# Performance work log

Hardware: AMD Instinct MI355X
Metric: run time of the kernel (lower is better)

Reference implementation:

```python
import jax, jax.numpy as jnp
import numpy as np

B, T, C, H = 4, 2048, 1024, 16
D = C // H  # head_dim = 64
SCALE = 1.0 / np.sqrt(D).astype(np.float32)


def setup_inputs() -> dict:
    key = jax.random.key(0)
    k1, k2, k3 = jax.random.split(key, 3)
    x = jax.random.normal(k1, (B, T, C), dtype=jnp.float32)
    Wqkv = jax.random.normal(k2, (C, 3 * C), dtype=jnp.float32) * (1.0 / np.sqrt(C))
    Wo = jax.random.normal(k3, (C, C), dtype=jnp.float32) * (1.0 / np.sqrt(C))
    bo = jnp.zeros((C,), dtype=jnp.float32)
    # causal mask, broadcastable [1,1,T,T]; positions where mask==0 get -inf
    mask = jnp.tril(jnp.ones((T, T), dtype=jnp.int32))[None, None]
    return {"x": x, "mask": mask, "Wqkv": Wqkv, "Wo": Wo, "bo": bo}


def reference(x, mask, Wqkv, Wo, bo):
    Bx, Tx, Cx = x.shape
    qkv = x @ Wqkv                               # [B, T, 3C]
    q, k, v = jnp.split(qkv, 3, axis=-1)
    # [B, T, C] -> [B, H, T, D]
    def heads(t):
        return t.reshape(Bx, Tx, H, D).transpose(0, 2, 1, 3)
    q, k, v = heads(q), heads(k), heads(v)
    scores = jnp.einsum('bhqd,bhkd->bhqk', q, k) * SCALE   # [B, H, T, T]
    scores = jnp.where(mask == 0, -jnp.inf, scores)
    attn = jax.nn.softmax(scores, axis=-1)
    out = jnp.einsum('bhqk,bhkd->bhqd', attn, v)           # [B, H, T, D]
    out = out.transpose(0, 2, 1, 3).reshape(Bx, Tx, Cx)    # [B, T, C]
    return out @ Wo + bo
```

## Files before the change

### kernel.cpp

```cpp
#include <hip/hip_runtime.h>

typedef __attribute__((ext_vector_type(8))) short short8;
typedef __attribute__((ext_vector_type(4))) float f32x4;
typedef __attribute__((ext_vector_type(4))) unsigned short ushort4v;

#define QK_PRESCALE 0.18033688011112043f
#define DEFER_THR 11.5f

__device__ __forceinline__ unsigned short f2bf(float f) {
    union { float f; unsigned int u; } v; v.f = f;
    unsigned int r = v.u + 0x7FFFu + ((v.u >> 16) & 1u);
    return (unsigned short)(r >> 16);
}

__global__ __launch_bounds__(256) void cvt_bf16(const float* __restrict__ in,
                                                unsigned short* __restrict__ out, int n) {
    int i = (blockIdx.x * 256 + threadIdx.x) * 4;
    if (i >= n) return;
    f32x4 v = *(const f32x4*)(in + i);
    ushort4v o;
    o[0] = f2bf(v[0]); o[1] = f2bf(v[1]); o[2] = f2bf(v[2]); o[3] = f2bf(v[3]);
    *(ushort4v*)(out + i) = o;
}

__global__ __launch_bounds__(256) void transpose_cvt(const float* __restrict__ W,
                                                     unsigned short* __restrict__ WT,
                                                     int Kd, int Nd) {
    __shared__ float tile[32][33];
    int n0 = blockIdx.x * 32, k0 = blockIdx.y * 32;
    int tx = threadIdx.x, ty = threadIdx.y;
    #pragma unroll
    for (int i = 0; i < 4; ++i)
        tile[ty + i * 8][tx] = W[(size_t)(k0 + ty + i * 8) * Nd + n0 + tx];
    __syncthreads();
    #pragma unroll
    for (int i = 0; i < 4; ++i) {
        int r = ty + i * 8;
        WT[(size_t)(n0 + r) * Kd + k0 + tx] = f2bf(tile[tx][r]);
    }
}

#define AS1U(p) ((const __attribute__((address_space(1))) unsigned int*)(p))
#define AS3U(p) ((__attribute__((address_space(3))) unsigned int*)(p))

template<int BIAS, int OUTBF16, int QSCALE>
__global__ __launch_bounds__(256) void gemm_bt(const unsigned short* __restrict__ A,
                                               const unsigned short* __restrict__ BT,
                                               void* __restrict__ Cv,
                                               const float* __restrict__ bias,
                                               int M, int N, int K) {
    __shared__ unsigned short As[128 * 32];
    __shared__ unsigned short Bs[128 * 32];
    int tid = threadIdx.x;
    int l = tid & 63, l15 = l & 15, l4 = l >> 4;
    int w = tid >> 6, wm = w >> 1, wn = w & 1;
    int bm = blockIdx.x, bn = blockIdx.y;

    f32x4 acc[4][4];
    #pragma unroll
    for (int mt = 0; mt < 4; ++mt)
        #pragma unroll
        for (int nt = 0; nt < 4; ++nt)
            acc[mt][nt] = (f32x4){0.f, 0.f, 0.f, 0.f};

    int srow = tid >> 2;
    int skk  = (tid & 3) * 8;

    const unsigned short* Ab = A  + (size_t)(bm * 128) * K;
    const unsigned short* Bb = BT + (size_t)(bn * 128) * K;

    for (int kt = 0; kt < K; kt += 32) {
        __syncthreads();
        __builtin_amdgcn_global_load_lds(AS1U(Ab + (size_t)srow        * K + kt + skk), AS3U(&As[tid * 8]),         16, 0, 0);
        __builtin_amdgcn_global_load_lds(AS1U(Ab + (size_t)(srow + 64) * K + kt + skk), AS3U(&As[(256 + tid) * 8]), 16, 0, 0);
        __builtin_amdgcn_global_load_lds(AS1U(Bb + (size_t)srow        * K + kt + skk), AS3U(&Bs[tid * 8]),         16, 0, 0);
        __builtin_amdgcn_global_load_lds(AS1U(Bb + (size_t)(srow + 64) * K + kt + skk), AS3U(&Bs[(256 + tid) * 8]), 16, 0, 0);
        __syncthreads();

        short8 av[4], bv[4];
        #pragma unroll
        for (int mt = 0; mt < 4; ++mt)
            av[mt] = *(const short8*)&As[(wm * 64 + mt * 16 + l15) * 32 + l4 * 8];
        #pragma unroll
        for (int nt = 0; nt < 4; ++nt)
            bv[nt] = *(const short8*)&Bs[(wn * 64 + nt * 16 + l15) * 32 + l4 * 8];
        #pragma unroll
        for (int mt = 0; mt < 4; ++mt)
            #pragma unroll
            for (int nt = 0; nt < 4; ++nt)
                acc[mt][nt] = __builtin_amdgcn_mfma_f32_16x16x32_bf16(av[mt], bv[nt], acc[mt][nt], 0, 0, 0);
    }

    #pragma unroll
    for (int mt = 0; mt < 4; ++mt) {
        #pragma unroll
        for (int r = 0; r < 4; ++r) {
            int row = bm * 128 + wm * 64 + mt * 16 + l4 * 4 + r;
            #pragma unroll
            for (int nt = 0; nt < 4; ++nt) {
                int col = bn * 128 + wn * 64 + nt * 16 + l15;
                float vv = acc[mt][nt][r];
                if (BIAS) vv += bias[col];
                if (QSCALE && col < 1024) vv *= QK_PRESCALE;
                if (OUTBF16) ((unsigned short*)Cv)[(size_t)row * N + col] = f2bf(vv);
                else         ((float*)Cv)[(size_t)row * N + col] = vv;
            }
        }
    }
}

__device__ __forceinline__ int swz64(int row, int e) {
    return row * 64 + (e ^ ((row & 7) << 3));
}

__global__ __launch_bounds__(256) void flash_attn(const unsigned short* __restrict__ qk,
                                                  const unsigned short* __restrict__ vt,
                                                  unsigned short* __restrict__ ao) {
    int nid = (blockIdx.x & 7) * 128 + (blockIdx.x >> 3);
    int pr = nid & 15;
    int bh = nid >> 4;
    int b = bh >> 4, h = bh & 15;
    int tid = threadIdx.x;
    int w = tid >> 6, l = tid & 63, l15 = l & 15, l4 = l >> 4;

    __shared__ unsigned short Ks[2][4096];
    __shared__ unsigned short Vs[2][4096];
    __shared__ unsigned short Ps[4096];

    const size_t qkbase = (size_t)b * 2048 * 2048;

    int c0i = w * 128 + l;
    int row0 = c0i >> 3, sub0 = c0i & 7;
    int c1i = c0i + 64;
    int row1 = c1i >> 3, sub1 = c1i & 7;

    const unsigned short* Kp0b = qk + qkbase + 1024 + h * 64 + (size_t)row0 * 2048 + 8 * (sub0 ^ (row0 & 7));
    const unsigned short* Kp1b = qk + qkbase + 1024 + h * 64 + (size_t)row1 * 2048 + 8 * (sub1 ^ (row1 & 7));
    const unsigned short* Vp0b = vt + (size_t)(h * 64 + row0) * 8192 + (size_t)b * 2048 + 8 * (sub0 ^ (row0 & 7));
    const unsigned short* Vp1b = vt + (size_t)(h * 64 + row1) * 8192 + (size_t)b * 2048 + 8 * (sub1 ^ (row1 & 7));

    #define STAGE(buf, kvb_)                                                                        \
        do {                                                                                        \
            size_t koff = (size_t)(kvb_) * (64 * 2048);                                             \
            int    voff = (kvb_) * 64;                                                              \
            __builtin_amdgcn_global_load_lds(AS1U(Kp0b + koff), AS3U(&Ks[buf][w * 1024]),       16, 0, 0); \
            __builtin_amdgcn_global_load_lds(AS1U(Kp1b + koff), AS3U(&Ks[buf][w * 1024 + 512]), 16, 0, 0); \
            __builtin_amdgcn_global_load_lds(AS1U(Vp0b + voff), AS3U(&Vs[buf][w * 1024]),       16, 0, 0); \
            __builtin_amdgcn_global_load_lds(AS1U(Vp1b + voff), AS3U(&Vs[buf][w * 1024 + 512]), 16, 0, 0); \
        } while (0)

    #pragma unroll
    for (int t = 0; t < 2; ++t) {
        int qt = t ? (31 - pr) : pr;

        int qrow = qt * 64 + w * 16 + l15;
        const unsigned short* qp = qk + qkbase + (size_t)qrow * 2048 + h * 64 + l4 * 8;
        short8 qa0 = *(const short8*)(qp);
        short8 qa1 = *(const short8*)(qp + 32);

        float m[4], ll[4];
        f32x4 oacc[4];
        #pragma unroll
        for (int r = 0; r < 4; ++r) { m[r] = -__builtin_inff(); ll[r] = 0.f; }
        #pragma unroll
        for (int dt = 0; dt < 4; ++dt) oacc[dt] = (f32x4){0.f, 0.f, 0.f, 0.f};

        STAGE(0, 0);
        __syncthreads();

        int cur = 0;
        for (int kvb = 0; kvb <= qt; ++kvb) {
            if (kvb < qt) STAGE(cur ^ 1, kvb + 1);

            f32x4 sacc[4];
            __builtin_amdgcn_s_setprio(1);
            #pragma unroll
            for (int kvt = 0; kvt < 4; ++kvt) {
                short8 k0v = *(const short8*)&Ks[cur][swz64(kvt * 16 + l15, l4 * 8)];
                short8 k1v = *(const short8*)&Ks[cur][swz64(kvt * 16 + l15, 32 + l4 * 8)];
                sacc[kvt] = (f32x4){0.f, 0.f, 0.f, 0.f};
                sacc[kvt] = __builtin_amdgcn_mfma_f32_16x16x32_bf16(qa0, k0v, sacc[kvt], 0, 0, 0);
                sacc[kvt] = __builtin_amdgcn_mfma_f32_16x16x32_bf16(qa1, k1v, sacc[kvt], 0, 0, 0);
            }
            __builtin_amdgcn_s_setprio(0);

            if (kvb == qt) {
                #pragma unroll
                for (int kvt = 0; kvt < 4; ++kvt)
                    #pragma unroll
                    for (int r = 0; r < 4; ++r) {
                        int ql = w * 16 + l4 * 4 + r;
                        int kl = kvt * 16 + l15;
                        if (kl > ql) sacc[kvt][r] = -__builtin_inff();
                    }
            }

            #pragma unroll
            for (int r = 0; r < 4; ++r) {
                float tmax = fmaxf(fmaxf(sacc[0][r], sacc[1][r]), fmaxf(sacc[2][r], sacc[3][r]));
                tmax = fmaxf(tmax, __shfl_xor(tmax, 1));
                tmax = fmaxf(tmax, __shfl_xor(tmax, 2));
                tmax = fmaxf(tmax, __shfl_xor(tmax, 4));
                tmax = fmaxf(tmax, __shfl_xor(tmax, 8));
                bool skip = (tmax <= m[r] + DEFER_THR);
                float mn = skip ? m[r] : tmax;
                float rsum = 0.f;
                #pragma unroll
                for (int kvt = 0; kvt < 4; ++kvt) {
                    float p = exp2f(sacc[kvt][r] - mn);
                    sacc[kvt][r] = p;
                    rsum += p;
                }
                rsum += __shfl_xor(rsum, 1);
                rsum += __shfl_xor(rsum, 2);
                rsum += __shfl_xor(rsum, 4);
                rsum += __shfl_xor(rsum, 8);
                if (skip) {
                    ll[r] += rsum;
                } else {
                    float alpha = exp2f(m[r] - mn);
                    ll[r] = ll[r] * alpha + rsum;
                    m[r] = mn;
                    #pragma unroll
                    for (int dt = 0; dt < 4; ++dt) oacc[dt][r] *= alpha;
                }
            }

            #pragma unroll
            for (int kvt = 0; kvt < 4; ++kvt)
                #pragma unroll
                for (int r = 0; r < 4; ++r)
                    Ps[w * 1024 + swz64(l4 * 4 + r, kvt * 16 + l15)] = f2bf(sacc[kvt][r]);
            short8 pa0 = *(const short8*)&Ps[w * 1024 + swz64(l15, l4 * 8)];
            short8 pa1 = *(const short8*)&Ps[w * 1024 + swz64(l15, 32 + l4 * 8)];

            __builtin_amdgcn_s_setprio(1);
            #pragma unroll
            for (int dt = 0; dt < 4; ++dt) {
                short8 vb0 = *(const short8*)&Vs[cur][swz64(dt * 16 + l15, l4 * 8)];
                short8 vb1 = *(const short8*)&Vs[cur][swz64(dt * 16 + l15, 32 + l4 * 8)];
                oacc[dt] = __builtin_amdgcn_mfma_f32_16x16x32_bf16(pa0, vb0, oacc[dt], 0, 0, 0);
                oacc[dt] = __builtin_amdgcn_mfma_f32_16x16x32_bf16(pa1, vb1, oacc[dt], 0, 0, 0);
            }
            __builtin_amdgcn_s_setprio(0);

            __syncthreads();
            cur ^= 1;
        }

        #pragma unroll
        for (int r = 0; r < 4; ++r) {
            float inv = 1.0f / ll[r];
            int row = qt * 64 + w * 16 + l4 * 4 + r;
            unsigned short* op = ao + ((size_t)b * 2048 + row) * 1024 + h * 64;
            #pragma unroll
            for (int dt = 0; dt < 4; ++dt)
                op[dt * 16 + l15] = f2bf(oacc[dt][r] * inv);
        }
    }
    #undef STAGE
}

extern "C" void kernel_launch(void* const* d_in, const int* in_sizes, int n_in,
                              void* d_out, int out_size, void* d_ws, size_t ws_size,
                              hipStream_t stream) {
    const float* x    = (const float*)d_in[0];
    const float* Wqkv = (const float*)d_in[2];
    const float* Wo   = (const float*)d_in[3];
    const float* bo   = (const float*)d_in[4];
    float* out = (float*)d_out;

    char* ws = (char*)d_ws;
    unsigned short* xb    = (unsigned short*)(ws);
    unsigned short* wqkvt = (unsigned short*)(ws + 16777216);
    unsigned short* wot   = (unsigned short*)(ws + 23068672);
    unsigned short* qkb   = (unsigned short*)(ws + 25165824);
    unsigned short* vtb   = (unsigned short*)(ws + 58720256);
    unsigned short* ao    = (unsigned short*)(ws + 75497472);

    cvt_bf16<<<8192, 256, 0, stream>>>(x, xb, 8192 * 1024);
    transpose_cvt<<<dim3(96, 32), dim3(32, 8), 0, stream>>>(Wqkv, wqkvt, 1024, 3072);
    transpose_cvt<<<dim3(32, 32), dim3(32, 8), 0, stream>>>(Wo, wot, 1024, 1024);

    gemm_bt<0, 1, 1><<<dim3(64, 16), 256, 0, stream>>>(xb, wqkvt, (void*)qkb, nullptr, 8192, 2048, 1024);
    gemm_bt<0, 1, 0><<<dim3(8, 64), 256, 0, stream>>>(wqkvt + (size_t)2048 * 1024, xb, (void*)vtb, nullptr, 1024, 8192, 1024);

    flash_attn<<<dim3(1024), 256, 0, stream>>>(qkb, vtb, ao);

    gemm_bt<1, 0, 0><<<dim3(64, 8), 256, 0, stream>>>(ao, wot, (void*)out, bo, 8192, 1024, 1024);
}
```

Before: 395.7 us.

## Compute transposed S tile so each lane owns one query row in softmax

Swaps the MFMA operands in the QK^T product so the score tile comes out transposed, with each lane holding a single query row. Row max and row sum then need only two cross-lane shuffles instead of four per row, and the running max and sum become scalars. The P tile is written to LDS with 4-wide vector stores instead of scalar stores. The output rescale now needs a shuffle to fetch each row's alpha, and that is done only when some lane's max changed.

```diff
diff --git a/kernel.cpp b/kernel.cpp
--- a/kernel.cpp
+++ b/kernel.cpp
@@ -1,6 +1,7 @@
 #include <hip/hip_runtime.h>
 
 typedef __attribute__((ext_vector_type(8))) short short8;
+typedef __attribute__((ext_vector_type(4))) short short4v;
 typedef __attribute__((ext_vector_type(4))) float f32x4;
 typedef __attribute__((ext_vector_type(4))) unsigned short ushort4v;
 
@@ -158,10 +159,8 @@
         short8 qa0 = *(const short8*)(qp);
         short8 qa1 = *(const short8*)(qp + 32);
 
-        float m[4], ll[4];
+        float mrow = -__builtin_inff(), llrow = 0.f;
         f32x4 oacc[4];
-        #pragma unroll
-        for (int r = 0; r < 4; ++r) { m[r] = -__builtin_inff(); ll[r] = 0.f; }
         #pragma unroll
         for (int dt = 0; dt < 4; ++dt) oacc[dt] = (f32x4){0.f, 0.f, 0.f, 0.f};
 
@@ -179,58 +178,68 @@
                 short8 k0v = *(const short8*)&Ks[cur][swz64(kvt * 16 + l15, l4 * 8)];
                 short8 k1v = *(const short8*)&Ks[cur][swz64(kvt * 16 + l15, 32 + l4 * 8)];
                 sacc[kvt] = (f32x4){0.f, 0.f, 0.f, 0.f};
-                sacc[kvt] = __builtin_amdgcn_mfma_f32_16x16x32_bf16(qa0, k0v, sacc[kvt], 0, 0, 0);
-                sacc[kvt] = __builtin_amdgcn_mfma_f32_16x16x32_bf16(qa1, k1v, sacc[kvt], 0, 0, 0);
+                sacc[kvt] = __builtin_amdgcn_mfma_f32_16x16x32_bf16(k0v, qa0, sacc[kvt], 0, 0, 0);
+                sacc[kvt] = __builtin_amdgcn_mfma_f32_16x16x32_bf16(k1v, qa1, sacc[kvt], 0, 0, 0);
             }
             __builtin_amdgcn_s_setprio(0);
 
             if (kvb == qt) {
+                int ql = w * 16 + l15;
                 #pragma unroll
                 for (int kvt = 0; kvt < 4; ++kvt)
                     #pragma unroll
                     for (int r = 0; r < 4; ++r) {
-                        int ql = w * 16 + l4 * 4 + r;
-                        int kl = kvt * 16 + l15;
+                        int kl = kvt * 16 + l4 * 4 + r;
                         if (kl > ql) sacc[kvt][r] = -__builtin_inff();
                     }
             }
 
-            #pragma unroll
-            for (int r = 0; r < 4; ++r) {
-                float tmax = fmaxf(fmaxf(sacc[0][r], sacc[1][r]), fmaxf(sacc[2][r], sacc[3][r]));
-                tmax = fmaxf(tmax, __shfl_xor(tmax, 1));
-                tmax = fmaxf(tmax, __shfl_xor(tmax, 2));
-                tmax = fmaxf(tmax, __shfl_xor(tmax, 4));
-                tmax = fmaxf(tmax, __shfl_xor(tmax, 8));
-                bool skip = (tmax <= m[r] + DEFER_THR);
-                float mn = skip ? m[r] : tmax;
-                float rsum = 0.f;
+            float tmax = sacc[0][0];
+            #pragma unroll
+            for (int kvt = 0; kvt < 4; ++kvt)
                 #pragma unroll
-                for (int kvt = 0; kvt < 4; ++kvt) {
+                for (int r = 0; r < 4; ++r)
+                    tmax = fmaxf(tmax, sacc[kvt][r]);
+            tmax = fmaxf(tmax, __shfl_xor(tmax, 16));
+            tmax = fmaxf(tmax, __shfl_xor(tmax, 32));
+
+            bool skip = (tmax <= mrow + DEFER_THR);
+            float mn = skip ? mrow : tmax;
+            float alphaL = skip ? 1.f : exp2f(mrow - mn);
+
+            float rsum = 0.f;
+            #pragma unroll
+            for (int kvt = 0; kvt < 4; ++kvt)
+                #pragma unroll
+                for (int r = 0; r < 4; ++r) {
                     float p = exp2f(sacc[kvt][r] - mn);
                     sacc[kvt][r] = p;
                     rsum += p;
                 }
-                rsum += __shfl_xor(rsum, 1);
-                rsum += __shfl_xor(rsum, 2);
-                rsum += __shfl_xor(rsum, 4);
-                rsum += __shfl_xor(rsum, 8);
-                if (skip) {
-                    ll[r] += rsum;
-                } else {
-                    float alpha = exp2f(m[r] - mn);
-                    ll[r] = ll[r] * alpha + rsum;
-                    m[r] = mn;
+            rsum += __shfl_xor(rsum, 16);
+            rsum += __shfl_xor(rsum, 32);
+
+            llrow = llrow * alphaL + rsum;
+            mrow = mn;
+
+            if (__any(!skip)) {
+                #pragma unroll
+                for (int r = 0; r < 4; ++r) {
+                    float aO = __shfl(alphaL, l4 * 4 + r);
                     #pragma unroll
-                    for (int dt = 0; dt < 4; ++dt) oacc[dt][r] *= alpha;
+                    for (int dt = 0; dt < 4; ++dt) oacc[dt][r] *= aO;
                 }
             }
 
             #pragma unroll
-            for (int kvt = 0; kvt < 4; ++kvt)
-                #pragma unroll
-                for (int r = 0; r < 4; ++r)
-                    Ps[w * 1024 + swz64(l4 * 4 + r, kvt * 16 + l15)] = f2bf(sacc[kvt][r]);
+            for (int kvt = 0; kvt < 4; ++kvt) {
+                short4v pk;
+                pk[0] = (short)f2bf(sacc[kvt][0]);
+                pk[1] = (short)f2bf(sacc[kvt][1]);
+                pk[2] = (short)f2bf(sacc[kvt][2]);
+                pk[3] = (short)f2bf(sacc[kvt][3]);
+                *(short4v*)&Ps[w * 1024 + swz64(l15, kvt * 16 + l4 * 4)] = pk;
+            }
             short8 pa0 = *(const short8*)&Ps[w * 1024 + swz64(l15, l4 * 8)];
             short8 pa1 = *(const short8*)&Ps[w * 1024 + swz64(l15, 32 + l4 * 8)];
 
@@ -250,7 +259,8 @@
 
         #pragma unroll
         for (int r = 0; r < 4; ++r) {
-            float inv = 1.0f / ll[r];
+            float llO = __shfl(llrow, l4 * 4 + r);
+            float inv = 1.0f / llO;
             int row = qt * 64 + w * 16 + l4 * 4 + r;
             unsigned short* op = ao + ((size_t)b * 2048 + row) * 1024 + h * 64;
             #pragma unroll
```

Result: faster. 318.5 us (-19.5%).
